# Kernel tuning notes

Hardware: AMD Instinct MI355X
Metric: run time of the kernel (lower is better)

Reference implementation:

```python
import jax, jax.numpy as jnp
import numpy as np

PATCH = 16
CH = 3


def setup_inputs() -> dict:
    key = jax.random.key(0)
    k1, k2, k3 = jax.random.split(key, 3)
    B, H = 16, 512
    embed_dim = PATCH * PATCH * CH  # 768
    x = jax.random.normal(k1, (B, CH, H, H), dtype=jnp.float32)
    fan_in = CH * PATCH * PATCH
    w = jax.random.normal(k2, (embed_dim, CH, PATCH, PATCH), dtype=jnp.float32) / np.float32(np.sqrt(fan_in))
    b = jax.random.normal(k3, (embed_dim,), dtype=jnp.float32) * 0.01
    return {"x": x, "w": w, "b": b}


def reference(x, w, b):
    p = w.shape[2]                      # patch_size
    B, C, imgsize, _ = x.shape
    pn = imgsize // p                   # patch_num (NOTE: pre-padding count, as in source)
    # zero-pad by one patch on every side
    xp = jnp.pad(x, ((0, 0), (0, 0), (p, p), (p, p)))
    # strided patch-embed conv: [B, embed_dim, pn+2, pn+2]
    xt = jax.lax.conv_general_dilated(xp, w, window_strides=(p, p), padding='VALID')
    xt = xt + b[None, :, None, None]
    B1, C1, H1, W1 = xt.shape           # H1 = W1 = pn + 2
    xt = xt.reshape(B1, C1, H1 * W1)
    # same (buggy-looking but faithful) index set / stride-pn neighbors as the source
    idxs = jnp.array([i * pn + j for i in range(1, pn - 1) for j in range(1, pn)], dtype=jnp.int32)
    inv8 = jnp.float32(1.0 / 8.0)

    def body(buf, idx):
        # torch aliases x_final=x_temp, so reads see earlier in-place writes -> sequential scan
        s = (buf[:, :, idx - pn] + buf[:, :, idx + pn]
             + buf[:, :, idx - 1] + buf[:, :, idx + 1]
             + buf[:, :, idx - pn - 1] + buf[:, :, idx - pn + 1]
             + buf[:, :, idx + pn - 1] + buf[:, :, idx + pn + 1]) * inv8
        return buf.at[:, :, idx].set(s), None

    xf, _ = jax.lax.scan(body, xt, idxs)
    side = imgsize + 2 * p              # embed_dim*H1*W1 == C*side*side by construction
    out = xf.reshape(B1, C, side, side)
    return out[:, :, p:imgsize + p, p:imgsize + p]
```

## Files before the change

### kernel.cpp

```cpp
#include <hip/hip_runtime.h>
#include <hip/hip_bf16.h>


typedef __attribute__((ext_vector_type(8))) short s8v;
typedef __attribute__((ext_vector_type(4))) float f4v;
typedef __attribute__((ext_vector_type(8))) unsigned short us8;
typedef __attribute__((ext_vector_type(4))) unsigned short us4;

__device__ __forceinline__ unsigned short f2bf(float f) {
    __hip_bfloat16 h = __float2bfloat16(f);
    return *reinterpret_cast<unsigned short*>(&h);
}
__device__ __forceinline__ float bf2f(unsigned short u) {
    union { unsigned int i; float f; } c; c.i = (unsigned int)u << 16; return c.f;
}

__global__ __launch_bounds__(256) void prep_w_k(const float* __restrict__ w,
                                                unsigned short* __restrict__ w_bf) {
    int g = blockIdx.x * 256 + threadIdx.x;
    int f = g << 3;
    const float4 v0 = *(const float4*)(w + f);
    const float4 v1 = *(const float4*)(w + f + 4);
    us8 u;
    u[0] = f2bf(v0.x); u[1] = f2bf(v0.y); u[2] = f2bf(v0.z); u[3] = f2bf(v0.w);
    u[4] = f2bf(v1.x); u[5] = f2bf(v1.y); u[6] = f2bf(v1.z); u[7] = f2bf(v1.w);
    *(us8*)(w_bf + f) = u;
}

__global__ __launch_bounds__(512, 4) void conv_gemm_rs_k(const float* __restrict__ x,
                                                         const unsigned short* __restrict__ W,
                                                         const float* __restrict__ bias,
                                                         unsigned short* __restrict__ xt) {
    __shared__ __align__(16) unsigned short As[2][128 * 32];
    __shared__ __align__(16) unsigned short Bs[2][192 * 32];
    const int tid  = threadIdx.x;
    const int lane = tid & 63, wv = tid >> 6;
    const int wr = wv >> 2, wc = wv & 3;
    const int m0 = blockIdx.x << 7;
    const int n0 = blockIdx.y * 192;
    const int bb = m0 >> 10;
    const int ph0 = (m0 >> 5) & 31;

    const int arow = tid >> 2, ach = tid & 3;
    const int phl  = arow >> 5, pw = arow & 31;
    const int aoff = (arow << 5) + ((ach ^ ((arow >> 1) & 3)) << 3);
    const float* xbase = x + (size_t)bb * 786432 + (ph0 + phl) * 8192
                           + (ach >> 1) * 512 + (pw << 4) + ((ach & 1) << 3);

    const int brow = tid >> 1, bpair = tid & 1;
    const int bxr  = (brow >> 1) & 3;
    const int boff0 = (brow << 5) + ((((bpair << 1))     ^ bxr) << 3);
    const int boff1 = (brow << 5) + ((((bpair << 1) | 1) ^ bxr) << 3);
    const unsigned short* wbase = W + (size_t)(n0 + brow) * 768 + (bpair << 4);

    float4 xr_[2][2];
    us8    wf_[2][2];

    auto gload = [&](int s, int t) {
        const float* sp = xbase + (t >> 3) * 262144 + (t & 7) * 1024;
        xr_[s][0] = *(const float4*)(sp);
        xr_[s][1] = *(const float4*)(sp + 4);
        if (tid < 384) {
            const unsigned short* ws = wbase + (t << 5);
            wf_[s][0] = *(const us8*)(ws);
            wf_[s][1] = *(const us8*)(ws + 8);
        }
    };
    auto store = [&](int s, int buf) {
        us8 lo;
        lo[0]=f2bf(xr_[s][0].x); lo[1]=f2bf(xr_[s][0].y);
        lo[2]=f2bf(xr_[s][0].z); lo[3]=f2bf(xr_[s][0].w);
        lo[4]=f2bf(xr_[s][1].x); lo[5]=f2bf(xr_[s][1].y);
        lo[6]=f2bf(xr_[s][1].z); lo[7]=f2bf(xr_[s][1].w);
        *(us8*)(As[buf] + aoff) = lo;
        if (tid < 384) {
            *(us8*)(Bs[buf] + boff0) = wf_[s][0];
            *(us8*)(Bs[buf] + boff1) = wf_[s][1];
        }
    };

    f4v acc[4][3] = {};
    gload(0, 0);
    store(0, 0);
    __syncthreads();

    const int cq = lane >> 4, l15 = lane & 15;
    #pragma unroll
    for (int t = 0; t < 24; ++t) {
        const int p = t & 1;
        if (t < 23) gload(p ^ 1, t + 1);
        s8v a[4], b[3];
        #pragma unroll
        for (int mi = 0; mi < 4; ++mi) {
            int ra = (wr << 6) + (mi << 4) + l15;
            a[mi] = *(const s8v*)(As[p] + (ra << 5) + ((cq ^ ((ra >> 1) & 3)) << 3));
        }
        #pragma unroll
        for (int ni = 0; ni < 3; ++ni) {
            int rb = wc * 48 + (ni << 4) + l15;
            b[ni] = *(const s8v*)(Bs[p] + (rb << 5) + ((cq ^ ((rb >> 1) & 3)) << 3));
        }
        #pragma unroll
        for (int mi = 0; mi < 4; ++mi)
            #pragma unroll
            for (int ni = 0; ni < 3; ++ni)
                acc[mi][ni] = __builtin_amdgcn_mfma_f32_16x16x32_bf16(a[mi], b[ni], acc[mi][ni], 0, 0, 0);
        if (t < 23) store(p ^ 1, p ^ 1);
        __syncthreads();
    }

    #pragma unroll
    for (int mi = 0; mi < 4; ++mi) {
        int m  = m0 + (wr << 6) + (mi << 4) + (cq << 2);
        int ph = (m >> 5) & 31, pwm = m & 31;
        unsigned short* dst = xt + (((size_t)bb * 768) << 10) + (ph << 5) + pwm;
        #pragma unroll
        for (int ni = 0; ni < 3; ++ni) {
            int n = n0 + wc * 48 + (ni << 4) + l15;
            float bv = bias[n];
            us4 o;
            o[0] = f2bf(acc[mi][ni][0] + bv);
            o[1] = f2bf(acc[mi][ni][1] + bv);
            o[2] = f2bf(acc[mi][ni][2] + bv);
            o[3] = f2bf(acc[mi][ni][3] + bv);
            *(us4*)(dst + ((size_t)n << 10)) = o;
        }
    }
}

__global__ __launch_bounds__(256) void scan_emit_k(const unsigned short* __restrict__ xt,
                                                   const float* __restrict__ bias,
                                                   float* __restrict__ out) {
    const int grp = (blockIdx.x * 256 + threadIdx.x) >> 5;
    const int j   = threadIdx.x & 31;
    const int b   = grp / 768;
    const int c1  = grp - b * 768;
    const unsigned short* basep = xt + ((size_t)grp << 10);
    const float bias_c = bias[c1];
    float* baseo = out + (size_t)b * 786432 + (size_t)(c1 >> 8) * 262144;

    int rem = (c1 & 255) * 1156 + j;
    int ey  = rem / 544;
    int ex  = rem - ey * 544;
    int eo  = (ey - 16) * 512 + (ex - 16);

    auto estep = [&](float v) {
        if (((unsigned)(ex - 16) < 512u) & ((unsigned)(ey - 16) < 512u))
            baseo[eo] = v;
        ex += 32;
        int wrp = (ex >= 544);
        ex -= wrp ? 544 : 0;
        ey += wrp;
        eo += wrp ? 0 : 32;
    };
    auto sel = [&](int p) -> float {
        unsigned int h = (unsigned int)p / 34u;
        unsigned int w = (unsigned int)p - h * 34u;
        if ((h == 0u) | (h == 33u) | (w == 0u) | (w == 33u)) return bias_c;
        return bf2f(basep[(h - 1u) * 32u + (w - 1u)]);
    };

    float co = sel( 32 + j);
    float no = sel( 64 + j);
    float o2 = sel( 96 + j);
    float o3 = sel(128 + j);
    estep(bias_c);
    float pn   = bias_c;
    float po_h = bias_c;
    float h_co = __shfl(co, 0, 32);
    float h_no = __shfl(no, 0, 32);
    float h_o2 = __shfl(o2, 0, 32);
    float rr   = __shfl_down(co, 1, 32);
    if (j == 31) rr = h_no;

    int pr  = 160 + j;
    int ph_ = pr / 34;
    int pw_ = pr - ph_ * 34;

    for (int i = 1; i <= 30; ++i) {
        bool bord = (pw_ == 0) | (pw_ == 33);
        float ld = bord ? bias_c : bf2f(basep[(ph_ - 1) * 32 + (pw_ - 1)]);
        pw_ += 32;
        if (pw_ >= 34) { pw_ -= 34; ++ph_; }

        float UL = __shfl_up(pn, 1, 32);   if (j == 1)  UL = po_h;
        float UR = __shfl_down(pn, 1, 32); if (j == 31) UR = h_co;
        float D1 = __shfl_up(no, 1, 32);
        float D3 = __shfl_down(no, 1, 32); if (j == 31) D3 = h_o2;
        float bv = (((UL + pn) + (UR + rr)) + ((D1 + no) + D3)) * 0.125f;
        if (j == 1) bv += h_co * 0.125f;
        float t;
        t = __shfl_up(bv, 1, 32);  bv += (j > 1) ? 0.125f * t : 0.f;
        t = __shfl_up(bv, 2, 32);  bv += (j > 2) ? 0.015625f * t : 0.f;
        estep((j == 0) ? co : bv);
        rr   = D3;
        pn   = bv;
        po_h = h_co; h_co = h_no; h_no = h_o2;
        h_o2 = __shfl(o3, 0, 32);
        co = no; no = o2; o2 = o3; o3 = ld;
    }
    estep(co);
    estep(no);
    estep(o2);
    estep(o3);
    estep(sel(1120 + j));
    if (j < 4) estep(bias_c);
}

extern "C" void kernel_launch(void* const* d_in, const int* in_sizes, int n_in,
                              void* d_out, int out_size, void* d_ws, size_t ws_size,
                              hipStream_t stream) {
    const float* x    = (const float*)d_in[0];
    const float* w    = (const float*)d_in[1];
    const float* bias = (const float*)d_in[2];
    float* out = (float*)d_out;
    unsigned short* xt = (unsigned short*)d_ws;

    unsigned short* w_bf = (unsigned short*)d_out;

    prep_w_k<<<288, 256, 0, stream>>>(w, w_bf);
    conv_gemm_rs_k<<<dim3(128, 4), 512, 0, stream>>>(x, w_bf, bias, xt);
    scan_emit_k<<<1536, 256, 0, stream>>>(xt, bias, out);
}
```

Measured before the change: 67.42 us.

## Switch conv GEMM to 32x32x16 MFMA with 128x128 tiles and 256 threads

The patch-embed GEMM moves from 16x16x32 bf16 MFMA on 128x192 tiles with 512 threads to 32x32x16 MFMA on 128x128 tiles with 4 waves. Each wave now computes a 64x64 sub-tile, and the grid grows to 128x6 blocks. The larger MFMA shape and the even load split, with no idle loader threads, are meant to cut LDS reads per flop and instruction overhead. The cost is 768 blocks instead of 512, different occupancy, and more accumulator registers per thread. The epilogue is rewritten to match the 32x32 accumulator layout.

```diff
diff --git a/kernel.cpp b/kernel.cpp
--- a/kernel.cpp
+++ b/kernel.cpp
@@ -2,10 +2,10 @@
 #include <hip/hip_bf16.h>
 
 
-typedef __attribute__((ext_vector_type(8))) short s8v;
-typedef __attribute__((ext_vector_type(4))) float f4v;
-typedef __attribute__((ext_vector_type(8))) unsigned short us8;
-typedef __attribute__((ext_vector_type(4))) unsigned short us4;
+typedef __attribute__((ext_vector_type(8)))  short s8v;
+typedef __attribute__((ext_vector_type(16))) float f16v;
+typedef __attribute__((ext_vector_type(8)))  unsigned short us8;
+typedef __attribute__((ext_vector_type(4)))  unsigned short us4;
 
 __device__ __forceinline__ unsigned short f2bf(float f) {
     __hip_bfloat16 h = __float2bfloat16(f);
@@ -27,103 +27,109 @@
     *(us8*)(w_bf + f) = u;
 }
 
-__global__ __launch_bounds__(512, 4) void conv_gemm_rs_k(const float* __restrict__ x,
+__global__ __launch_bounds__(256, 3) void conv_gemm_32_k(const float* __restrict__ x,
                                                          const unsigned short* __restrict__ W,
                                                          const float* __restrict__ bias,
                                                          unsigned short* __restrict__ xt) {
     __shared__ __align__(16) unsigned short As[2][128 * 32];
-    __shared__ __align__(16) unsigned short Bs[2][192 * 32];
+    __shared__ __align__(16) unsigned short Bs[2][128 * 32];
     const int tid  = threadIdx.x;
     const int lane = tid & 63, wv = tid >> 6;
-    const int wr = wv >> 2, wc = wv & 3;
-    const int m0 = blockIdx.x << 7;
-    const int n0 = blockIdx.y * 192;
+    const int wr = wv >> 1, wc = wv & 1;
+    const int m0 = blockIdx.x << 7, n0 = blockIdx.y << 7;
     const int bb = m0 >> 10;
     const int ph0 = (m0 >> 5) & 31;
 
-    const int arow = tid >> 2, ach = tid & 3;
-    const int phl  = arow >> 5, pw = arow & 31;
-    const int aoff = (arow << 5) + ((ach ^ ((arow >> 1) & 3)) << 3);
-    const float* xbase = x + (size_t)bb * 786432 + (ph0 + phl) * 8192
-                           + (ach >> 1) * 512 + (pw << 4) + ((ach & 1) << 3);
-
-    const int brow = tid >> 1, bpair = tid & 1;
-    const int bxr  = (brow >> 1) & 3;
-    const int boff0 = (brow << 5) + ((((bpair << 1))     ^ bxr) << 3);
-    const int boff1 = (brow << 5) + ((((bpair << 1) | 1) ^ bxr) << 3);
-    const unsigned short* wbase = W + (size_t)(n0 + brow) * 768 + (bpair << 4);
-
-    float4 xr_[2][2];
+    int u0 = tid, u1 = tid + 256;
+    int r0 = u0 >> 2, c0 = u0 & 3, r1 = u1 >> 2, c1u = u1 & 3;
+    const int aoff0 = (r0 << 5) + ((c0  ^ ((r0 >> 1) & 3)) << 3);
+    const int aoff1 = (r1 << 5) + ((c1u ^ ((r1 >> 1) & 3)) << 3);
+    const float* xb0 = x + (size_t)bb * 786432 + (ph0 + (r0 >> 5)) * 8192
+                         + (c0 >> 1) * 512 + ((r0 & 31) << 4) + ((c0 & 1) << 3);
+    const float* xb1 = x + (size_t)bb * 786432 + (ph0 + (r1 >> 5)) * 8192
+                         + (c1u >> 1) * 512 + ((r1 & 31) << 4) + ((c1u & 1) << 3);
+    const unsigned short* wb0 = W + (size_t)(n0 + r0) * 768 + (c0 << 3);
+    const unsigned short* wb1 = W + (size_t)(n0 + r1) * 768 + (c1u << 3);
+
+    float4 xr_[2][2][2];
     us8    wf_[2][2];
 
     auto gload = [&](int s, int t) {
-        const float* sp = xbase + (t >> 3) * 262144 + (t & 7) * 1024;
-        xr_[s][0] = *(const float4*)(sp);
-        xr_[s][1] = *(const float4*)(sp + 4);
-        if (tid < 384) {
-            const unsigned short* ws = wbase + (t << 5);
-            wf_[s][0] = *(const us8*)(ws);
-            wf_[s][1] = *(const us8*)(ws + 8);
-        }
+        const int ko = (t >> 3) * 262144 + (t & 7) * 1024;
+        xr_[s][0][0] = *(const float4*)(xb0 + ko);
+        xr_[s][0][1] = *(const float4*)(xb0 + ko + 4);
+        xr_[s][1][0] = *(const float4*)(xb1 + ko);
+        xr_[s][1][1] = *(const float4*)(xb1 + ko + 4);
+        wf_[s][0] = *(const us8*)(wb0 + (t << 5));
+        wf_[s][1] = *(const us8*)(wb1 + (t << 5));
     };
     auto store = [&](int s, int buf) {
-        us8 lo;
-        lo[0]=f2bf(xr_[s][0].x); lo[1]=f2bf(xr_[s][0].y);
-        lo[2]=f2bf(xr_[s][0].z); lo[3]=f2bf(xr_[s][0].w);
-        lo[4]=f2bf(xr_[s][1].x); lo[5]=f2bf(xr_[s][1].y);
-        lo[6]=f2bf(xr_[s][1].z); lo[7]=f2bf(xr_[s][1].w);
-        *(us8*)(As[buf] + aoff) = lo;
-        if (tid < 384) {
-            *(us8*)(Bs[buf] + boff0) = wf_[s][0];
-            *(us8*)(Bs[buf] + boff1) = wf_[s][1];
-        }
-    };
-
-    f4v acc[4][3] = {};
+        us8 o0, o1;
+        o0[0]=f2bf(xr_[s][0][0].x); o0[1]=f2bf(xr_[s][0][0].y);
+        o0[2]=f2bf(xr_[s][0][0].z); o0[3]=f2bf(xr_[s][0][0].w);
+        o0[4]=f2bf(xr_[s][0][1].x); o0[5]=f2bf(xr_[s][0][1].y);
+        o0[6]=f2bf(xr_[s][0][1].z); o0[7]=f2bf(xr_[s][0][1].w);
+        o1[0]=f2bf(xr_[s][1][0].x); o1[1]=f2bf(xr_[s][1][0].y);
+        o1[2]=f2bf(xr_[s][1][0].z); o1[3]=f2bf(xr_[s][1][0].w);
+        o1[4]=f2bf(xr_[s][1][1].x); o1[5]=f2bf(xr_[s][1][1].y);
+        o1[6]=f2bf(xr_[s][1][1].z); o1[7]=f2bf(xr_[s][1][1].w);
+        *(us8*)(As[buf] + aoff0) = o0;
+        *(us8*)(As[buf] + aoff1) = o1;
+        *(us8*)(Bs[buf] + aoff0) = wf_[s][0];
+        *(us8*)(Bs[buf] + aoff1) = wf_[s][1];
+    };
+
+    f16v acc[2][2] = {};
     gload(0, 0);
     store(0, 0);
     __syncthreads();
 
-    const int cq = lane >> 4, l15 = lane & 15;
+    const int l31 = lane & 31, khi = lane >> 5;
     #pragma unroll
     for (int t = 0; t < 24; ++t) {
         const int p = t & 1;
         if (t < 23) gload(p ^ 1, t + 1);
-        s8v a[4], b[3];
+        s8v a[2][2], b[2][2];
         #pragma unroll
-        for (int mi = 0; mi < 4; ++mi) {
-            int ra = (wr << 6) + (mi << 4) + l15;
-            a[mi] = *(const s8v*)(As[p] + (ra << 5) + ((cq ^ ((ra >> 1) & 3)) << 3));
-        }
+        for (int mi = 0; mi < 2; ++mi)
+            #pragma unroll
+            for (int kh = 0; kh < 2; ++kh) {
+                int ra = (wr << 6) + (mi << 5) + l31;
+                int ca = (kh << 1) + khi;
+                a[mi][kh] = *(const s8v*)(As[p] + (ra << 5) + ((ca ^ ((ra >> 1) & 3)) << 3));
+                int rb = (wc << 6) + (mi << 5) + l31;
+                b[mi][kh] = *(const s8v*)(Bs[p] + (rb << 5) + ((ca ^ ((rb >> 1) & 3)) << 3));
+            }
         #pragma unroll
-        for (int ni = 0; ni < 3; ++ni) {
-            int rb = wc * 48 + (ni << 4) + l15;
-            b[ni] = *(const s8v*)(Bs[p] + (rb << 5) + ((cq ^ ((rb >> 1) & 3)) << 3));
-        }
-        #pragma unroll
-        for (int mi = 0; mi < 4; ++mi)
+        for (int kh = 0; kh < 2; ++kh)
             #pragma unroll
-            for (int ni = 0; ni < 3; ++ni)
-                acc[mi][ni] = __builtin_amdgcn_mfma_f32_16x16x32_bf16(a[mi], b[ni], acc[mi][ni], 0, 0, 0);
+            for (int mi = 0; mi < 2; ++mi)
+                #pragma unroll
+                for (int ni = 0; ni < 2; ++ni)
+                    acc[mi][ni] = __builtin_amdgcn_mfma_f32_32x32x16_bf16(
+                        a[mi][kh], b[ni][kh], acc[mi][ni], 0, 0, 0);
         if (t < 23) store(p ^ 1, p ^ 1);
         __syncthreads();
     }
 
     #pragma unroll
-    for (int mi = 0; mi < 4; ++mi) {
-        int m  = m0 + (wr << 6) + (mi << 4) + (cq << 2);
-        int ph = (m >> 5) & 31, pwm = m & 31;
-        unsigned short* dst = xt + (((size_t)bb * 768) << 10) + (ph << 5) + pwm;
+    for (int ni = 0; ni < 2; ++ni) {
+        int n = n0 + (wc << 6) + (ni << 5) + l31;
+        float bv = bias[n];
+        unsigned short* dstn = xt + (((size_t)bb * 768 + n) << 10);
         #pragma unroll
-        for (int ni = 0; ni < 3; ++ni) {
-            int n = n0 + wc * 48 + (ni << 4) + l15;
-            float bv = bias[n];
-            us4 o;
-            o[0] = f2bf(acc[mi][ni][0] + bv);
-            o[1] = f2bf(acc[mi][ni][1] + bv);
-            o[2] = f2bf(acc[mi][ni][2] + bv);
-            o[3] = f2bf(acc[mi][ni][3] + bv);
-            *(us4*)(dst + ((size_t)n << 10)) = o;
+        for (int mi = 0; mi < 2; ++mi) {
+            #pragma unroll
+            for (int g = 0; g < 4; ++g) {
+                int m  = m0 + (wr << 6) + (mi << 5) + (g << 3) + (khi << 2);
+                int ph = (m >> 5) & 31, pwm = m & 31;
+                us4 o;
+                o[0] = f2bf(acc[mi][ni][4 * g + 0] + bv);
+                o[1] = f2bf(acc[mi][ni][4 * g + 1] + bv);
+                o[2] = f2bf(acc[mi][ni][4 * g + 2] + bv);
+                o[3] = f2bf(acc[mi][ni][4 * g + 3] + bv);
+                *(us4*)(dstn + (ph << 5) + pwm) = o;
+            }
         }
     }
 }
@@ -219,6 +225,6 @@
     unsigned short* w_bf = (unsigned short*)d_out;
 
     prep_w_k<<<288, 256, 0, stream>>>(w, w_bf);
-    conv_gemm_rs_k<<<dim3(128, 4), 512, 0, stream>>>(x, w_bf, bias, xt);
+    conv_gemm_32_k<<<dim3(128, 6), 256, 0, stream>>>(x, w_bf, bias, xt);
     scan_emit_k<<<1536, 256, 0, stream>>>(xt, bias, out);
 }
```

Result: slower. 74.00 us (+9.8%).
